# Kernel tuning notes

Hardware: AMD Instinct MI355X
Metric: run time of the kernel (lower is better)

Reference implementation:

```python
import jax, jax.numpy as jnp
import numpy as np

B, H, V, A, NANN, DEPTH = 32, 256, 512, 3, 8, 7


def preorder_perm(arity, depth):
    # level-order node index -> pre-order position permutation for a full arity-ary tree
    starts = np.cumsum([0] + [arity ** l for l in range(depth + 1)])
    order = []
    def rec(l, p):
        order.append(int(starts[l] + p))
        if l < depth:
            for c in range(arity):
                rec(l + 1, p * arity + c)
    rec(0, 0)
    return np.asarray(order, dtype=np.int32)


def setup_inputs() -> dict:
    key = jax.random.key(0)
    ks = jax.random.split(key, 12)
    s = 0.05
    return {
        "root_hiddens": jax.random.normal(ks[0], (B, H), jnp.float32),
        "ann_table": jax.random.normal(ks[1], (NANN, H), jnp.float32),
        "w1": jax.random.normal(ks[2], (2 * H, H), jnp.float32) * s,
        "b1": jnp.zeros((2 * H,), jnp.float32),
        "w2": jax.random.normal(ks[3], (V, 2 * H), jnp.float32) * s,
        "b2": jnp.zeros((V,), jnp.float32),
        "gru_w_ih": jax.random.normal(ks[4], (A, 3 * H, H), jnp.float32) * s,
        "gru_w_hh": jax.random.normal(ks[5], (A, 3 * H, H), jnp.float32) * s,
        "gru_b_ih": jnp.zeros((A, 3 * H), jnp.float32),
        "gru_b_hh": jnp.zeros((A, 3 * H), jnp.float32),
        "ann_ids": jax.random.randint(ks[6], (B,), 0, NANN, jnp.int32),
        "depth": DEPTH,
    }


def _forward(root_hiddens, ann_table, w1, b1, w2, b2,
             gru_w_ih, gru_w_hh, gru_b_ih, gru_b_hh, ann_ids, depth):
    b, h = root_hiddens.shape
    arity = gru_w_ih.shape[0]
    x = ann_table[ann_ids]                                   # [B,H] annotation embedding (GRU input at every node)
    # input-side gates are constant across the whole tree: precompute once
    gx = jnp.einsum('bh,agh->bag', x, gru_w_ih) + gru_b_ih   # [B,A,3H]
    xr, xz, xn = jnp.split(gx, 3, axis=-1)                   # each [B,A,H]

    hid = root_hiddens[:, None, :]                           # [B,1,H]
    levels = [hid]
    for _ in range(depth):
        gh = jnp.einsum('bnh,agh->bnag', hid, gru_w_hh) + gru_b_hh  # [B,n,A,3H]
        hr, hz, hn = jnp.split(gh, 3, axis=-1)
        r = jax.nn.sigmoid(xr[:, None] + hr)
        z = jax.nn.sigmoid(xz[:, None] + hz)
        n = jnp.tanh(xn[:, None] + r * hn)
        new_h = (1.0 - z) * n + z * hid[:, :, None, :]       # [B,n,A,H]
        hid = new_h.reshape(b, -1, h)                        # child c of node p -> p*A+c
        levels.append(hid)

    all_h = jnp.concatenate(levels, axis=1)                  # [B,N,H] level-order
    mid = jax.nn.sigmoid(jnp.einsum('bnh,oh->bno', all_h, w1) + b1)
    prod = jnp.einsum('bno,vo->bnv', mid, w2) + b2           # [B,N,V]
    perm = jnp.asarray(preorder_perm(arity, depth))
    return jnp.transpose(prod[:, perm, :], (1, 0, 2))        # [N,B,V] (seq-first, like pad_sequence)


def reference(root_hiddens, ann_table, w1, b1, w2, b2,
              gru_w_ih, gru_w_hh, gru_b_ih, gru_b_hh, ann_ids, depth):
    return _forward(root_hiddens, ann_table, w1, b1, w2, b2,
                    gru_w_ih, gru_w_hh, gru_b_ih, gru_b_hh, ann_ids, depth)
```

## Files before the change

kernel.cpp:

```cpp
#include <hip/hip_runtime.h>
#include <hip/hip_bf16.h>
#include <stdint.h>
#include <stddef.h>

#define NB 32
#define NH 256
#define NMID 512
#define NV 512
#define NA 3
#define NDEPTH 7
#define NNODES 3280
#define NG 2304
#define MROWS (NNODES * NB)
#define HM 64

typedef __attribute__((ext_vector_type(8))) short bf16x8;
typedef __attribute__((ext_vector_type(4))) float f32x4;

__device__ __forceinline__ unsigned short f2bf(float x) {
    union { float f; unsigned u; } v; v.f = x;
    unsigned r = v.u + 0x7fffu + ((v.u >> 16) & 1u);
    return (unsigned short)(r >> 16);
}
__device__ __forceinline__ unsigned cvt_pk_bf16(float a, float b) {
    unsigned r;
    asm("v_cvt_pk_bf16_f32 %0, %1, %2" : "=v"(r) : "v"(a), "v"(b));
    return r;
}
__device__ __forceinline__ float bf2f(unsigned short u) {
    union { unsigned u; float f; } v; v.u = ((unsigned)u) << 16;
    return v.f;
}
__device__ __forceinline__ float sigm(float x) { return 1.0f / (1.0f + __expf(-x)); }
__device__ __forceinline__ float tanh_(float x) {
    x = fminf(fmaxf(x, -15.0f), 15.0f);
    float e = __expf(2.0f * x);
    return (e - 1.0f) / (e + 1.0f);
}
__device__ __forceinline__ f32x4 splat4(float s) { f32x4 v = {s, s, s, s}; return v; }

__device__ __forceinline__ int preorder_pos(int n) {
    int start = 0, cnt = 1, l = 0;
    while (n >= start + cnt) { start += cnt; cnt *= 3; l++; }
    int p = n - start;
    int pw = 1;
    for (int j = 0; j < l - 1; j++) pw *= 3;
    int pos = 0;
    for (int k = 1; k <= l; k++) {
        int d = (p / pw) % 3;
        int e = NDEPTH - k + 1;
        int p3 = 1; for (int j = 0; j < e; j++) p3 *= 3;
        pos += 1 + d * ((p3 - 1) / 2);
        pw /= 3;
    }
    return pos;
}

__global__ void prep_all(const float* __restrict__ root, const float* __restrict__ ann_table,
                         const int* __restrict__ ann_ids,
                         const float* __restrict__ w_ih, const float* __restrict__ b_ih,
                         const float* __restrict__ whh_f, const float* __restrict__ w1_f,
                         const float* __restrict__ w2_f,
                         unsigned short* __restrict__ whh_b, unsigned short* __restrict__ w1_b,
                         unsigned short* __restrict__ w2_b,
                         float* __restrict__ gx_t, int* __restrict__ posmap,
                         unsigned short* __restrict__ hid_b) {
    int gtid = blockIdx.x * blockDim.x + threadIdx.x;
    int nth = gridDim.x * blockDim.x;
    const int n_whh = NG * NH, n_w1 = NMID * NH, n_w2 = NV * NMID;
    const int total = n_whh + n_w1 + n_w2;
    for (int i = gtid; i < total; i += nth) {
        if (i < n_whh) whh_b[i] = f2bf(whh_f[i]);
        else if (i < n_whh + n_w1) w1_b[i - n_whh] = f2bf(w1_f[i - n_whh]);
        else w2_b[i - n_whh - n_w1] = f2bf(w2_f[i - n_whh - n_w1]);
    }
    if (gtid < NB * NH) hid_b[gtid] = f2bf(root[gtid]);
    if (gtid < NNODES) posmap[gtid] = preorder_pos(gtid);
    int lane = threadIdx.x & 63;
    int gw = gtid >> 6;
    int nw = nth >> 6;
    for (int e = gw; e < NB * NG; e += nw) {
        int b = e / NG;
        int col = e - b * NG;
        const float* xr = ann_table + (size_t)ann_ids[b] * NH;
        const float* wr = w_ih + (size_t)col * NH;
        float4 xv = *(const float4*)(xr + lane * 4);
        float4 wv = *(const float4*)(wr + lane * 4);
        float s = xv.x * wv.x + xv.y * wv.y + xv.z * wv.z + xv.w * wv.w;
        #pragma unroll
        for (int off = 32; off; off >>= 1) s += __shfl_down(s, off);
        if (lane == 0) gx_t[(size_t)col * NB + b] = s + b_ih[col];
    }
}

template<int NPB>
__global__ __launch_bounds__(512, 2)
void gru_level(const unsigned short* __restrict__ hid_b_in,
               unsigned short* __restrict__ hid_b_out,
               const unsigned short* __restrict__ whh_b,
               const float* __restrict__ b_hh, const float* __restrict__ gx_t,
               int start, int child_start, int cnt) {
    constexpr int M = 32 * NPB;
    __shared__ char a_s[M * 512];

    int tid = threadIdx.x;
    int lane = tid & 63;
    int wv = tid >> 6;
    int lr = lane & 15;
    int kg = (lane >> 4) * 8;
    int rbase = (lane >> 4) * 4;
    int nrel0 = blockIdx.x * NPB;
    size_t prow0 = (size_t)(start + nrel0) * NB;

    for (int c = tid; c < M * 32; c += 512) {
        int row = c >> 5;
        int coloff = (c & 31) * 8;
        bf16x8 v = *(const bf16x8*)(hid_b_in + (prow0 + row) * NH + coloff);
        *(bf16x8*)(a_s + ((row * 512 + coloff * 2) ^ ((row & 15) << 4))) = v;
    }
    __syncthreads();

    int Gb = (blockIdx.y * 8 + wv) * 16;
    int a = Gb >> 8;
    int colh = (Gb & 255) + lr;
    int gcol = a * 768 + colh;
    const unsigned short* bptr = whh_b + (size_t)(a * 512 + Gb + lr) * NH + kg;

    float bhr = b_hh[gcol], bhz = b_hh[gcol + 256], bhn = b_hh[gcol + 512];

    f32x4 acc[3][2 * NPB];
    #pragma unroll
    for (int g = 0; g < 2; ++g) {
        f32x4 gr = *(const f32x4*)(gx_t + (size_t)gcol * NB + g * 16 + rbase);
        f32x4 gz = *(const f32x4*)(gx_t + (size_t)(gcol + 256) * NB + g * 16 + rbase);
        #pragma unroll
        for (int mi = g; mi < 2 * NPB; mi += 2) {
            acc[0][mi] = gr + splat4(bhr);
            acc[1][mi] = gz + splat4(bhz);
            acc[2][mi] = splat4(bhn);
        }
    }

    bf16x8 bcur[3];
    #pragma unroll
    for (int t = 0; t < 3; ++t) bcur[t] = *(const bf16x8*)(bptr + t * 256 * NH);
    #pragma unroll
    for (int k0 = 0; k0 < NH; k0 += 32) {
        bf16x8 bnxt[3];
        if (k0 + 32 < NH) {
            #pragma unroll
            for (int t = 0; t < 3; ++t) bnxt[t] = *(const bf16x8*)(bptr + t * 256 * NH + k0 + 32);
        }
        bf16x8 af[2 * NPB];
        #pragma unroll
        for (int mi = 0; mi < 2 * NPB; ++mi) {
            int row = mi * 16 + lr;
            af[mi] = *(const bf16x8*)(a_s + ((row * 512 + (k0 + kg) * 2) ^ ((row & 15) << 4)));
        }
        #pragma unroll
        for (int t = 0; t < 3; ++t)
            #pragma unroll
            for (int mi = 0; mi < 2 * NPB; ++mi)
                acc[t][mi] = __builtin_amdgcn_mfma_f32_16x16x32_bf16(af[mi], bcur[t], acc[t][mi], 0, 0, 0);
        if (k0 + 32 < NH) {
            #pragma unroll
            for (int t = 0; t < 3; ++t) bcur[t] = bnxt[t];
        }
    }

    f32x4 gxn[2];
    #pragma unroll
    for (int g = 0; g < 2; ++g)
        gxn[g] = *(const f32x4*)(gx_t + (size_t)(gcol + 512) * NB + g * 16 + rbase);
    #pragma unroll
    for (int mi = 0; mi < 2 * NPB; ++mi) {
        int ns = (mi * 16 + rbase) >> 5;
        if (nrel0 + ns >= cnt) continue;
        size_t crow = ((size_t)(child_start + (nrel0 + ns) * 3 + a)) * NB;
        float hnew[4];
        #pragma unroll
        for (int j = 0; j < 4; ++j) {
            int row = mi * 16 + rbase + j;
            float r = sigm(acc[0][mi][j]);
            float z = sigm(acc[1][mi][j]);
            float nn = tanh_(gxn[mi & 1][j] + r * acc[2][mi][j]);
            unsigned short hpu = *(const unsigned short*)(a_s + ((row * 512 + colh * 2) ^ ((row & 15) << 4)));
            hnew[j] = (1.0f - z) * nn + z * bf2f(hpu);
        }
        unsigned u01 = cvt_pk_bf16(hnew[0], hnew[1]);
        unsigned u23 = cvt_pk_bf16(hnew[2], hnew[3]);
        int b0 = (mi * 16 + rbase) & 31;
        hid_b_out[(crow + b0 + 0) * NH + colh] = (unsigned short)u01;
        hid_b_out[(crow + b0 + 1) * NH + colh] = (unsigned short)(u01 >> 16);
        hid_b_out[(crow + b0 + 2) * NH + colh] = (unsigned short)u23;
        hid_b_out[(crow + b0 + 3) * NH + colh] = (unsigned short)(u23 >> 16);
    }
}

__global__ __launch_bounds__(512, 4)
void head_fused(const unsigned short* __restrict__ hid_b,
                const unsigned short* __restrict__ w1_b, const float* __restrict__ b1,
                const unsigned short* __restrict__ w2_b, const float* __restrict__ b2,
                const int* __restrict__ posmap, float* __restrict__ out) {
    __shared__ char smem[HM * NMID * 2];

    int tid = threadIdx.x;
    int lane = tid & 63;
    int wv = tid >> 6;
    int mbase = blockIdx.x * HM;
    int lr = lane & 15;
    int kg = (lane >> 4) * 8;
    int rbase = (lane >> 4) * 4;
    int n0w = wv * 64;

    for (int c = tid; c < HM * 32; c += 512) {
        int row = c >> 5;
        int coloff = (c & 31) * 8;
        bf16x8 v = *(const bf16x8*)(hid_b + ((size_t)(mbase + row)) * NH + coloff);
        *(bf16x8*)(smem + ((row * 512 + coloff * 2) ^ ((row & 15) << 4))) = v;
    }
    __syncthreads();

    f32x4 acc[4][4];
    #pragma unroll
    for (int mi = 0; mi < 4; ++mi)
        #pragma unroll
        for (int ni = 0; ni < 4; ++ni) acc[mi][ni] = (f32x4){0.f, 0.f, 0.f, 0.f};

    {
        const unsigned short* bbase = w1_b + ((size_t)(n0w + lr)) * NH + kg;
        bf16x8 bcur[4];
        #pragma unroll
        for (int ni = 0; ni < 4; ++ni) bcur[ni] = *(const bf16x8*)(bbase + ni * 16 * NH);
        #pragma unroll
        for (int k0 = 0; k0 < NH; k0 += 32) {
            bf16x8 bnxt[4];
            if (k0 + 32 < NH) {
                #pragma unroll
                for (int ni = 0; ni < 4; ++ni) bnxt[ni] = *(const bf16x8*)(bbase + ni * 16 * NH + k0 + 32);
            }
            bf16x8 af[4];
            #pragma unroll
            for (int mi = 0; mi < 4; ++mi) {
                int row = mi * 16 + lr;
                af[mi] = *(const bf16x8*)(smem + ((row * 512 + (k0 + kg) * 2) ^ ((row & 15) << 4)));
            }
            #pragma unroll
            for (int mi = 0; mi < 4; ++mi)
                #pragma unroll
                for (int ni = 0; ni < 4; ++ni)
                    acc[mi][ni] = __builtin_amdgcn_mfma_f32_16x16x32_bf16(af[mi], bcur[ni], acc[mi][ni], 0, 0, 0);
            if (k0 + 32 < NH) {
                #pragma unroll
                for (int ni = 0; ni < 4; ++ni) bcur[ni] = bnxt[ni];
            }
        }
    }
    __syncthreads();

    #pragma unroll
    for (int mi = 0; mi < 4; ++mi)
        #pragma unroll
        for (int ni = 0; ni < 4; ++ni) {
            int col = n0w + ni * 16 + lr;
            float bv = b1[col];
            float v0 = sigm(acc[mi][ni][0] + bv);
            float v1 = sigm(acc[mi][ni][1] + bv);
            float v2 = sigm(acc[mi][ni][2] + bv);
            float v3 = sigm(acc[mi][ni][3] + bv);
            unsigned u01 = cvt_pk_bf16(v0, v1);
            unsigned u23 = cvt_pk_bf16(v2, v3);
            int r0 = mi * 16 + rbase;
            *(unsigned short*)(smem + (((r0 + 0) * 1024 + col * 2) ^ (((r0 + 0) & 15) << 4))) = (unsigned short)u01;
            *(unsigned short*)(smem + (((r0 + 1) * 1024 + col * 2) ^ (((r0 + 1) & 15) << 4))) = (unsigned short)(u01 >> 16);
            *(unsigned short*)(smem + (((r0 + 2) * 1024 + col * 2) ^ (((r0 + 2) & 15) << 4))) = (unsigned short)u23;
            *(unsigned short*)(smem + (((r0 + 3) * 1024 + col * 2) ^ (((r0 + 3) & 15) << 4))) = (unsigned short)(u23 >> 16);
        }
    __syncthreads();

    #pragma unroll
    for (int mi = 0; mi < 4; ++mi)
        #pragma unroll
        for (int ni = 0; ni < 4; ++ni) acc[mi][ni] = (f32x4){0.f, 0.f, 0.f, 0.f};
    {
        const unsigned short* bbase = w2_b + ((size_t)(n0w + lr)) * NMID + kg;
        bf16x8 bcur[4];
        #pragma unroll
        for (int ni = 0; ni < 4; ++ni) bcur[ni] = *(const bf16x8*)(bbase + ni * 16 * NMID);
        #pragma unroll
        for (int k0 = 0; k0 < NMID; k0 += 32) {
            bf16x8 bnxt[4];
            if (k0 + 32 < NMID) {
                #pragma unroll
                for (int ni = 0; ni < 4; ++ni) bnxt[ni] = *(const bf16x8*)(bbase + ni * 16 * NMID + k0 + 32);
            }
            bf16x8 af[4];
            #pragma unroll
            for (int mi = 0; mi < 4; ++mi) {
                int row = mi * 16 + lr;
                af[mi] = *(const bf16x8*)(smem + ((row * 1024 + (k0 + kg) * 2) ^ ((row & 15) << 4)));
            }
            #pragma unroll
            for (int mi = 0; mi < 4; ++mi)
                #pragma unroll
                for (int ni = 0; ni < 4; ++ni)
                    acc[mi][ni] = __builtin_amdgcn_mfma_f32_16x16x32_bf16(af[mi], bcur[ni], acc[mi][ni], 0, 0, 0);
            if (k0 + 32 < NMID) {
                #pragma unroll
                for (int ni = 0; ni < 4; ++ni) bcur[ni] = bnxt[ni];
            }
        }
    }
    __syncthreads();

    float bv4[4];
    #pragma unroll
    for (int ni = 0; ni < 4; ++ni) bv4[ni] = b2[n0w + ni * 16 + lr];
    #pragma unroll
    for (int h = 0; h < 2; ++h) {
        #pragma unroll
        for (int mm = 0; mm < 2; ++mm) {
            int mi = h * 2 + mm;
            #pragma unroll
            for (int ni = 0; ni < 4; ++ni) {
                int col = n0w + ni * 16 + lr;
                #pragma unroll
                for (int j = 0; j < 4; ++j) {
                    int rl = mm * 16 + rbase + j;
                    int byteoff = (rl * 2048 + col * 4) ^ ((rl & 7) << 4);
                    *(float*)(smem + byteoff) = acc[mi][ni][j] + bv4[ni];
                }
            }
        }
        __syncthreads();
        int pos = posmap[blockIdx.x * 2 + h];
        float* obase = out + (size_t)pos * NB * NV;
        #pragma unroll
        for (int i = 0; i < 8; ++i) {
            int f = tid + i * 512;
            int rl = f >> 7;
            int cq = f & 127;
            int byteoff = (rl * 2048 + cq * 16) ^ ((rl & 7) << 4);
            f32x4 v = *(const f32x4*)(smem + byteoff);
            *(f32x4*)(obase + (size_t)rl * NV + cq * 4) = v;
        }
        if (h == 0) __syncthreads();
    }
}

extern "C" void kernel_launch(void* const* d_in, const int* in_sizes, int n_in,
                              void* d_out, int out_size, void* d_ws, size_t ws_size,
                              hipStream_t stream) {
    const float* root      = (const float*)d_in[0];
    const float* ann_table = (const float*)d_in[1];
    const float* w1        = (const float*)d_in[2];
    const float* b1        = (const float*)d_in[3];
    const float* w2        = (const float*)d_in[4];
    const float* b2        = (const float*)d_in[5];
    const float* w_ih      = (const float*)d_in[6];
    const float* w_hh      = (const float*)d_in[7];
    const float* b_ih      = (const float*)d_in[8];
    const float* b_hh      = (const float*)d_in[9];
    const int*   ann_ids   = (const int*)d_in[10];

    uint8_t* ws = (uint8_t*)d_ws;
    unsigned short* whh_b = (unsigned short*)ws; ws += (size_t)NG * NH * 2;
    unsigned short* w1_b  = (unsigned short*)ws; ws += (size_t)NMID * NH * 2;
    unsigned short* w2_b  = (unsigned short*)ws; ws += (size_t)NV * NMID * 2;
    float* gx_t           = (float*)ws;          ws += (size_t)NB * NG * 4;
    int* posmap           = (int*)ws;            ws += (size_t)NNODES * 4;
    unsigned short* hid_b = (unsigned short*)ws; ws += (size_t)NNODES * NB * NH * 2;

    prep_all<<<1024, 256, 0, stream>>>(root, ann_table, ann_ids, w_ih, b_ih,
                                       w_hh, w1, w2, whh_b, w1_b, w2_b,
                                       gx_t, posmap, hid_b);

    int start = 0, cnt = 1;
    for (int l = 0; l < NDEPTH; ++l) {
        int child_start = start + cnt;
        if (cnt >= 243) {
            gru_level<4><<<dim3((cnt + 3) / 4, 6), 512, 0, stream>>>(
                hid_b, hid_b, whh_b, b_hh, gx_t, start, child_start, cnt);
        } else {
            gru_level<1><<<dim3(cnt, 6), 512, 0, stream>>>(
                hid_b, hid_b, whh_b, b_hh, gx_t, start, child_start, cnt);
        }
        start = child_start; cnt *= 3;
    }
    head_fused<<<MROWS / HM, 512, 0, stream>>>(hid_b, w1_b, b1, w2_b, b2, posmap, (float*)d_out);
}
```

Measured before the change: 377.6 us.

## Write head outputs directly from accumulators and tune GRU level dispatch

The head kernel epilogue now stores accumulator values plus bias straight to global memory through the posmap. This replaces staging them in shared memory for vectorized coalesced rows, which removes two block barriers and an LDS round trip but makes the stores narrower and less coalesced. The GRU level kernel raises wave priority around its MFMA block. A two-nodes-per-block variant is used for medium-sized levels, with the four-node variant reserved for the largest ones.

```diff
diff --git a/kernel.cpp b/kernel.cpp
--- a/kernel.cpp
+++ b/kernel.cpp
@@ -157,11 +157,13 @@
             int row = mi * 16 + lr;
             af[mi] = *(const bf16x8*)(a_s + ((row * 512 + (k0 + kg) * 2) ^ ((row & 15) << 4)));
         }
+        __builtin_amdgcn_s_setprio(1);
         #pragma unroll
         for (int t = 0; t < 3; ++t)
             #pragma unroll
             for (int mi = 0; mi < 2 * NPB; ++mi)
                 acc[t][mi] = __builtin_amdgcn_mfma_f32_16x16x32_bf16(af[mi], bcur[t], acc[t][mi], 0, 0, 0);
+        __builtin_amdgcn_s_setprio(0);
         if (k0 + 32 < NH) {
             #pragma unroll
             for (int t = 0; t < 3; ++t) bcur[t] = bnxt[t];
@@ -311,40 +313,22 @@
             }
         }
     }
-    __syncthreads();
-
     float bv4[4];
     #pragma unroll
     for (int ni = 0; ni < 4; ++ni) bv4[ni] = b2[n0w + ni * 16 + lr];
     #pragma unroll
-    for (int h = 0; h < 2; ++h) {
-        #pragma unroll
-        for (int mm = 0; mm < 2; ++mm) {
-            int mi = h * 2 + mm;
-            #pragma unroll
-            for (int ni = 0; ni < 4; ++ni) {
-                int col = n0w + ni * 16 + lr;
-                #pragma unroll
-                for (int j = 0; j < 4; ++j) {
-                    int rl = mm * 16 + rbase + j;
-                    int byteoff = (rl * 2048 + col * 4) ^ ((rl & 7) << 4);
-                    *(float*)(smem + byteoff) = acc[mi][ni][j] + bv4[ni];
-                }
-            }
-        }
-        __syncthreads();
-        int pos = posmap[blockIdx.x * 2 + h];
-        float* obase = out + (size_t)pos * NB * NV;
-        #pragma unroll
-        for (int i = 0; i < 8; ++i) {
-            int f = tid + i * 512;
-            int rl = f >> 7;
-            int cq = f & 127;
-            int byteoff = (rl * 2048 + cq * 16) ^ ((rl & 7) << 4);
-            f32x4 v = *(const f32x4*)(smem + byteoff);
-            *(f32x4*)(obase + (size_t)rl * NV + cq * 4) = v;
-        }
-        if (h == 0) __syncthreads();
+    for (int mi = 0; mi < 4; ++mi) {
+        int row0 = mbase + mi * 16 + rbase;
+        #pragma unroll
+        for (int j = 0; j < 4; ++j) {
+            int row = row0 + j;
+            int b = row & 31;
+            int node = row >> 5;
+            float* orow = out + ((size_t)posmap[node] * NB + b) * NV + n0w + lr;
+            #pragma unroll
+            for (int ni = 0; ni < 4; ++ni)
+                orow[ni * 16] = acc[mi][ni][j] + bv4[ni];
+        }
     }
 }
 
@@ -378,8 +362,11 @@
     int start = 0, cnt = 1;
     for (int l = 0; l < NDEPTH; ++l) {
         int child_start = start + cnt;
-        if (cnt >= 243) {
+        if (cnt >= 729) {
             gru_level<4><<<dim3((cnt + 3) / 4, 6), 512, 0, stream>>>(
+                hid_b, hid_b, whh_b, b_hh, gx_t, start, child_start, cnt);
+        } else if (cnt >= 128) {
+            gru_level<2><<<dim3((cnt + 1) / 2, 6), 512, 0, stream>>>(
                 hid_b, hid_b, whh_b, b_hh, gx_t, start, child_start, cnt);
         } else {
             gru_level<1><<<dim3(cnt, 6), 512, 0, stream>>>(
```

New measurement: 365.7 us. -3.1%, faster.
